# Kernel tuning notes

Hardware: AMD Instinct MI355X
Metric: run time of the kernel (lower is better)

Reference implementation:

```python
import jax, jax.numpy as jnp
import numpy as np

EPS = 1e-5

def layer_norm(x, gamma, beta):
    mu = jnp.mean(x, axis=-1, keepdims=True)
    var = jnp.var(x, axis=-1, keepdims=True)
    return (x - mu) * jax.lax.rsqrt(var + EPS) * gamma + beta

def setup_inputs() -> dict:
    key = jax.random.key(0)
    ks = jax.random.split(key, 8)
    T, B, E, H, K = 2048, 2, 1024, 16, 64
    x = jax.random.normal(ks[0], (T, B, E), dtype=jnp.float32)
    # causal mask: 0 where allowed (s<=t), -1e9 where masked
    attn_mask = jnp.where(jnp.tril(jnp.ones((T, T), dtype=bool)), 0.0, -1e9).astype(jnp.float32)
    def xavier(k, shape, gain):
        fan_out, fan_in = shape
        std = gain * np.sqrt(2.0 / (fan_in + fan_out))
        return (jax.random.normal(k, shape, dtype=jnp.float32) * std)
    Wq = xavier(ks[1], (H * K, E), 1.0)
    Wk = xavier(ks[2], (K, E), 1.0)
    Wv = xavier(ks[3], (E, E), 1.0)
    return {
        'x': x, 'attn_mask': attn_mask,
        'Wq': Wq, 'bq': jnp.zeros((H * K,), jnp.float32),
        'Wk': Wk, 'bk': jnp.zeros((K,), jnp.float32),
        'Wv': Wv, 'bv': jnp.zeros((E,), jnp.float32),
        'k_gamma': jnp.ones((K,), jnp.float32), 'k_beta': jnp.zeros((K,), jnp.float32),
        'v_gamma': jnp.ones((E,), jnp.float32), 'v_beta': jnp.zeros((E,), jnp.float32),
    }

def reference(x, attn_mask, Wq, bq, Wk, bk, Wv, bv, k_gamma, k_beta, v_gamma, v_beta):
    T, B, E = x.shape
    K = Wk.shape[0]
    H = Wq.shape[0] // K
    q = (x @ Wq.T + bq).reshape(T, B, H, K)          # [T,B,H,K]
    k = layer_norm(x @ Wk.T + bk, k_gamma, k_beta)   # [T,B,K]
    v = layer_norm(x @ Wv.T + bv, v_gamma, v_beta)   # [T,B,E]
    # outer-product state per step, then causal cumulative sum.
    # einsum('ts,sbkd->tbkd', scaling*causal_mask, s) == cumsum over s<=t,
    # scaled per query position t by (t+1)^-0.5 (mask is causal lower-tri).
    outer = jnp.einsum('tbk,tbd->tbkd', k, v)        # [T,B,K,E]
    s = jnp.cumsum(outer, axis=0)
    scaling = jax.lax.rsqrt(jnp.arange(1, T + 1, dtype=x.dtype))
    s = s * scaling[:, None, None, None]
    qn = jnp.mean(jax.nn.softmax(q, axis=-1), axis=2)  # [T,B,K] (dropout_p=0, eval)
    attn = jnp.einsum('tbk,tbkd->tbd', qn, s)          # [T,B,E]
    return attn
```

## Files before the change

### kernel.cpp

```cpp
#include <hip/hip_runtime.h>
#include <math.h>

#define T_DIM 2048
#define B_DIM 2
#define E_DIM 1024
#define K_DIM 64
#define H_DIM 16
#define R_DIM (T_DIM * B_DIM)
#define WROWS 2176
#define NCH 16

typedef __bf16 bf16x8 __attribute__((ext_vector_type(8)));
typedef __bf16 bf16x4 __attribute__((ext_vector_type(4)));
typedef float f32x4 __attribute__((ext_vector_type(4)));

#define GLD16(gptr, lptr)                                                      \
    __builtin_amdgcn_global_load_lds(                                          \
        (const __attribute__((address_space(1))) void*)(gptr),                 \
        (__attribute__((address_space(3))) void*)(lptr), 16, 0, 0)

__global__ __launch_bounds__(256) void cvt_all(const float* __restrict__ X,
                                               const float* __restrict__ Wq,
                                               const float* __restrict__ Wv,
                                               const float* __restrict__ Wk,
                                               __bf16* __restrict__ XB,
                                               __bf16* __restrict__ WB) {
    const size_t nq = (size_t)1024 * 1024;
    const size_t nk = (size_t)64 * 1024;
    bf16x8 o;
    if (blockIdx.x < 2048) {
        size_t g = ((size_t)blockIdx.x * 256 + threadIdx.x) * 8;
        float4 a = *(const float4*)&X[g];
        float4 b = *(const float4*)&X[g + 4];
        o[0] = (__bf16)a.x; o[1] = (__bf16)a.y; o[2] = (__bf16)a.z; o[3] = (__bf16)a.w;
        o[4] = (__bf16)b.x; o[5] = (__bf16)b.y; o[6] = (__bf16)b.z; o[7] = (__bf16)b.w;
        *(bf16x8*)&XB[g] = o;
    } else {
        size_t g = ((size_t)(blockIdx.x - 2048) * 256 + threadIdx.x) * 8;
        if (g < 2 * nq + nk) {
            const float* src;
            size_t off;
            if (g < nq)          { src = Wq; off = g; }
            else if (g < 2 * nq) { src = Wv; off = g - nq; }
            else                 { src = Wk; off = g - 2 * nq; }
            float4 a = *(const float4*)&src[off];
            float4 b = *(const float4*)&src[off + 4];
            o[0] = (__bf16)a.x; o[1] = (__bf16)a.y; o[2] = (__bf16)a.z; o[3] = (__bf16)a.w;
            o[4] = (__bf16)b.x; o[5] = (__bf16)b.y; o[6] = (__bf16)b.z; o[7] = (__bf16)b.w;
        } else {
#pragma unroll
            for (int i = 0; i < 8; ++i) o[i] = (__bf16)0.f;
        }
        *(bf16x8*)&WB[g] = o;
    }
}

__global__ __launch_bounds__(256) void gemm_mfma(const __bf16* __restrict__ XB,
                                                 const __bf16* __restrict__ WB,
                                                 const float* __restrict__ bq,
                                                 const float* __restrict__ bv,
                                                 const float* __restrict__ bk,
                                                 __bf16* __restrict__ Qb,
                                                 __bf16* __restrict__ Vb,
                                                 float* __restrict__ Kr) {
    __shared__ __bf16 Als[128 * 32];
    __shared__ __bf16 Bls[128 * 32];
    const int bid = blockIdx.x;
    const int v = (bid & 7) * 68 + (bid >> 3);
    const int bx = v / 17;
    const int by = v % 17;
    const int tid = threadIdx.x;
    const int lane = tid & 63;
    const int w = tid >> 6;
    const int wm = (w & 1) * 64;
    const int wn = (w >> 1) * 64;
    const int rBase = bx * 128;
    const int cBase = by * 128;

    const int c0 = tid, c1 = tid + 256;
    const __bf16* gA0 = XB + (size_t)(rBase + (c0 >> 2)) * E_DIM + (c0 & 3) * 8;
    const __bf16* gA1 = XB + (size_t)(rBase + (c1 >> 2)) * E_DIM + (c1 & 3) * 8;
    const __bf16* gB0 = WB + (size_t)(cBase + (c0 >> 2)) * E_DIM + (c0 & 3) * 8;
    const __bf16* gB1 = WB + (size_t)(cBase + (c1 >> 2)) * E_DIM + (c1 & 3) * 8;
    __bf16* lA0 = Als + c0 * 8;
    __bf16* lA1 = Als + c1 * 8;
    __bf16* lB0 = Bls + c0 * 8;
    __bf16* lB1 = Bls + c1 * 8;

    const int fr = lane & 15;
    const int fk = (lane >> 4) * 8;
    const __bf16* aF = Als + (wm + fr) * 32 + fk;
    const __bf16* bF = Bls + (wn + fr) * 32 + fk;

    f32x4 acc[4][4] = {};

    for (int kk = 0; kk < E_DIM; kk += 32) {
        __syncthreads();
        GLD16(gA0 + kk, lA0);
        GLD16(gA1 + kk, lA1);
        GLD16(gB0 + kk, lB0);
        GLD16(gB1 + kk, lB1);
        __syncthreads();

        bf16x8 af[4], bfr[4];
#pragma unroll
        for (int mt = 0; mt < 4; ++mt) af[mt] = *(const bf16x8*)(aF + mt * 16 * 32);
#pragma unroll
        for (int nt = 0; nt < 4; ++nt) bfr[nt] = *(const bf16x8*)(bF + nt * 16 * 32);
#pragma unroll
        for (int mt = 0; mt < 4; ++mt)
#pragma unroll
            for (int nt = 0; nt < 4; ++nt)
                acc[mt][nt] = __builtin_amdgcn_mfma_f32_16x16x32_bf16(
                    af[mt], bfr[nt], acc[mt][nt], 0, 0, 0);
    }

    const int row0 = rBase + wm + (lane >> 4) * 4;
    if (cBase < 2048) {
        const float* bias;
        __bf16* Cout;
        int colBase;
        if (cBase < 1024) { bias = bq; Cout = Qb; colBase = cBase; }
        else              { bias = bv; Cout = Vb; colBase = cBase - 1024; }
        const int col0 = colBase + wn + (lane & 15);
#pragma unroll
        for (int mt = 0; mt < 4; ++mt)
#pragma unroll
            for (int nt = 0; nt < 4; ++nt) {
                int cc = col0 + nt * 16;
                float bb = bias[cc];
#pragma unroll
                for (int r = 0; r < 4; ++r)
                    Cout[(size_t)(row0 + mt * 16 + r) * E_DIM + cc] =
                        (__bf16)(acc[mt][nt][r] + bb);
            }
    } else {
        const int col0 = wn + (lane & 15);
#pragma unroll
        for (int mt = 0; mt < 4; ++mt)
#pragma unroll
            for (int nt = 0; nt < 4; ++nt) {
                int cc = col0 + nt * 16;
                if (cc < 64) {
                    float bb = bk[cc];
#pragma unroll
                    for (int r = 0; r < 4; ++r)
                        Kr[(size_t)(row0 + mt * 16 + r) * K_DIM + cc] =
                            acc[mt][nt][r] + bb;
                }
            }
    }
}

__global__ __launch_bounds__(256) void rowops(const __bf16* __restrict__ Qb,
                                              const float* __restrict__ Kraw,
                                              const __bf16* __restrict__ Vb,
                                              const float* __restrict__ kg,
                                              const float* __restrict__ kb,
                                              __bf16* __restrict__ QNB,
                                              __bf16* __restrict__ KNB,
                                              float2* __restrict__ ST) {
    const int r = blockIdx.x;
    const int tid = threadIdx.x;
    const int lane = tid & 63, wv = tid >> 6;
    const int t = r >> 1, b = r & 1;
    __shared__ float redq[4][64];
    __shared__ float redv[2][4];

    float acc = 0.f;
#pragma unroll
    for (int h4 = 0; h4 < 4; ++h4) {
        int h = wv * 4 + h4;
        float v = (float)Qb[(size_t)r * 1024 + h * 64 + lane];
        float m = v;
#pragma unroll
        for (int off = 32; off; off >>= 1) m = fmaxf(m, __shfl_xor(m, off));
        float e = expf(v - m);
        float ssum = e;
#pragma unroll
        for (int off = 32; off; off >>= 1) ssum += __shfl_xor(ssum, off);
        acc += e / ssum;
    }
    redq[wv][lane] = acc;

    {
        bf16x4 v4 = *(const bf16x4*)&Vb[(size_t)r * 1024 + tid * 4];
        float a = (float)v4[0], c = (float)v4[1], d = (float)v4[2], e = (float)v4[3];
        float s = a + c + d + e;
        float s2 = a * a + c * c + d * d + e * e;
#pragma unroll
        for (int off = 32; off; off >>= 1) {
            s += __shfl_xor(s, off);
            s2 += __shfl_xor(s2, off);
        }
        if (lane == 0) { redv[0][wv] = s; redv[1][wv] = s2; }
    }
    __syncthreads();

    if (tid < 64) {
        float s = redq[0][tid] + redq[1][tid] + redq[2][tid] + redq[3][tid];
        QNB[((size_t)b * T_DIM + t) * K_DIM + tid] = (__bf16)(s * (1.f / 16.f));
    } else if (tid < 128) {
        float v = Kraw[(size_t)r * K_DIM + lane];
        float s = v, s2 = v * v;
#pragma unroll
        for (int off = 32; off; off >>= 1) {
            s += __shfl_xor(s, off);
            s2 += __shfl_xor(s2, off);
        }
        float mean = s * (1.f / 64.f);
        float var = s2 * (1.f / 64.f) - mean * mean;
        float inv = rsqrtf(var + 1e-5f);
        KNB[((size_t)b * T_DIM + t) * K_DIM + lane] =
            (__bf16)((v - mean) * inv * kg[lane] + kb[lane]);
    } else if (tid == 128) {
        float s = redv[0][0] + redv[0][1] + redv[0][2] + redv[0][3];
        float s2 = redv[1][0] + redv[1][1] + redv[1][2] + redv[1][3];
        float mean = s * (1.f / 1024.f);
        float var = s2 * (1.f / 1024.f) - mean * mean;
        ST[r] = make_float2(mean, rsqrtf(var + 1e-5f));
    }
}

__global__ __launch_bounds__(256) void lnT_stateU(const __bf16* __restrict__ VB,
                                                  const float2* __restrict__ ST,
                                                  const float* __restrict__ gamma,
                                                  const float* __restrict__ beta,
                                                  const __bf16* __restrict__ KNB,
                                                  __bf16* __restrict__ VT,
                                                  float* __restrict__ U) {
    __shared__ float tile[64][65];
    __shared__ __bf16 knT[64 * 136];
    __shared__ __bf16 VTl[64 * 136];
    const int c = blockIdx.x, b = blockIdx.y, eq = blockIdx.z;
    const int tid = threadIdx.x;
    const int lane = tid & 63;
    const int w = tid >> 6;
    const int fr = lane & 15;
    const int quad = lane >> 4;
    const int e0 = eq * 64;

    {
        int s = tid >> 1, kh = (tid & 1) * 32;
        const __bf16* src = KNB + ((size_t)b * T_DIM + c * 128 + s) * K_DIM + kh;
#pragma unroll
        for (int i8 = 0; i8 < 4; ++i8) {
            bf16x8 vv = *(const bf16x8*)&src[i8 * 8];
#pragma unroll
            for (int i = 0; i < 8; ++i) knT[(kh + i8 * 8 + i) * 136 + s] = vv[i];
        }
    }

#pragma unroll
    for (int th = 0; th < 2; ++th) {
#pragma unroll
        for (int j = 0; j < 2; ++j) {
            int idx = tid + j * 256;
            int tl = idx >> 3, e8 = idx & 7;
            int r = (c * 128 + th * 64 + tl) * B_DIM + b;
            float2 st = ST[r];
            bf16x8 vv = *(const bf16x8*)&VB[(size_t)r * E_DIM + e0 + e8 * 8];
#pragma unroll
            for (int i = 0; i < 8; ++i)
                tile[tl][e8 * 8 + i] = ((float)vv[i] - st.x) * st.y;
        }
        __syncthreads();
#pragma unroll
        for (int j = 0; j < 4; ++j) {
            int idx = tid + j * 256;
            int e = idx >> 4, t4 = idx & 15;
            float g = gamma[e0 + e], bb = beta[e0 + e];
            bf16x4 o;
#pragma unroll
            for (int i = 0; i < 4; ++i) o[i] = (__bf16)(tile[t4 * 4 + i][e] * g + bb);
            *(bf16x4*)&VT[((size_t)b * E_DIM + e0 + e) * T_DIM + c * 128 + th * 64 + t4 * 4] = o;
            *(bf16x4*)&VTl[e * 136 + th * 64 + t4 * 4] = o;
        }
        __syncthreads();
    }

    f32x4 acc[4] = {};
#pragma unroll
    for (int kit = 0; kit < 4; ++kit) {
        bf16x8 af = *(const bf16x8*)&VTl[(w * 16 + fr) * 136 + kit * 32 + quad * 8];
        bf16x8 bfr[4];
#pragma unroll
        for (int nt = 0; nt < 4; ++nt)
            bfr[nt] = *(const bf16x8*)&knT[(nt * 16 + fr) * 136 + kit * 32 + quad * 8];
#pragma unroll
        for (int nt = 0; nt < 4; ++nt)
            acc[nt] = __builtin_amdgcn_mfma_f32_16x16x32_bf16(
                af, bfr[nt], acc[nt], 0, 0, 0);
    }

    float* ub = U + ((size_t)(c * 2 + b) * 1024 + e0) * K_DIM;
#pragma unroll
    for (int nt = 0; nt < 4; ++nt) {
        int k = nt * 16 + fr;
#pragma unroll
        for (int r = 0; r < 4; ++r)
            ub[(size_t)(w * 16 + quad * 4 + r) * K_DIM + k] = acc[nt][r];
    }
}

__global__ __launch_bounds__(256) void scanS(const float* __restrict__ U,
                                             __bf16* __restrict__ Shi,
                                             __bf16* __restrict__ Slo) {
    const size_t idx = (size_t)blockIdx.x * 256 + threadIdx.x;
    float run = 0.f;
#pragma unroll
    for (int c = 0; c < NCH; ++c) {
        __bf16 h = (__bf16)run;
        Shi[(size_t)c * 131072 + idx] = h;
        Slo[(size_t)c * 131072 + idx] = (__bf16)(run - (float)h);
        run += U[(size_t)c * 131072 + idx];
    }
}

__global__ __launch_bounds__(256) void outPV(const __bf16* __restrict__ QNB,
                                             const __bf16* __restrict__ KNB,
                                             const __bf16* __restrict__ VT,
                                             const __bf16* __restrict__ Shi,
                                             const __bf16* __restrict__ Slo,
                                             float* __restrict__ OUT) {
    __shared__ __align__(16) __bf16 qns[128 * 72];
    __shared__ __align__(16) __bf16 Pl[128 * 136];
    __shared__ __align__(16) __bf16 Vls[128 * 32];
    const int c = blockIdx.x, b = blockIdx.y, eo = blockIdx.z;
    const int tid = threadIdx.x;
    const int lane = tid & 63;
    const int w = tid >> 6;
    const int fr = lane & 15;
    const int quad = lane >> 4;

#pragma unroll
    for (int j = 0; j < 4; ++j) {
        int idx = tid + j * 256;
        int row = idx >> 3, k8 = idx & 7;
        *(bf16x8*)&qns[row * 72 + k8 * 8] =
            *(const bf16x8*)&QNB[((size_t)b * T_DIM + c * 128 + row) * K_DIM + k8 * 8];
    }
    __syncthreads();

    const __bf16* knc = KNB + ((size_t)b * T_DIM + c * 128) * K_DIM;
    {
        f32x4 pacc[8][2] = {};
#pragma unroll
        for (int kit = 0; kit < 2; ++kit) {
            bf16x8 bq[2];
#pragma unroll
            for (int nt = 0; nt < 2; ++nt) {
                int q = w * 32 + nt * 16 + fr;
                bq[nt] = *(const bf16x8*)&qns[q * 72 + kit * 32 + quad * 8];
            }
#pragma unroll
            for (int mt = 0; mt < 8; ++mt) {
                bf16x8 af = *(const bf16x8*)&knc[(size_t)(mt * 16 + fr) * K_DIM +
                                                 kit * 32 + quad * 8];
#pragma unroll
                for (int nt = 0; nt < 2; ++nt)
                    pacc[mt][nt] = __builtin_amdgcn_mfma_f32_16x16x32_bf16(
                        af, bq[nt], pacc[mt][nt], 0, 0, 0);
            }
        }
#pragma unroll
        for (int mt = 0; mt < 8; ++mt)
#pragma unroll
            for (int nt = 0; nt < 2; ++nt) {
                int q = w * 32 + nt * 16 + fr;
                int s0 = mt * 16 + quad * 4;
                bf16x4 o;
#pragma unroll
                for (int r = 0; r < 4; ++r) {
                    float val = pacc[mt][nt][r];
                    if (s0 + r > q) val = 0.f;
                    o[r] = (__bf16)val;
                }
                *(bf16x4*)&Pl[q * 136 + s0] = o;
            }
    }
    __syncthreads();

    const int we = (w & 1) * 64, wt = (w >> 1) * 64;
    const int e0 = eo * 128;
    f32x4 acc[4][4] = {};

    if (c > 0) {
        const __bf16* sh = Shi + (size_t)c * 131072 + ((size_t)b * 1024 + e0 + we) * K_DIM;
        const __bf16* sl = Slo + (size_t)c * 131072 + ((size_t)b * 1024 + e0 + we) * K_DIM;
#pragma unroll
        for (int kit = 0; kit < 2; ++kit) {
            bf16x8 bq[4];
#pragma unroll
            for (int nt = 0; nt < 4; ++nt) {
                int t = wt + nt * 16 + fr;
                bq[nt] = *(const bf16x8*)&qns[t * 72 + kit * 32 + quad * 8];
            }
#pragma unroll
            for (int mt = 0; mt < 4; ++mt) {
                size_t ro = (size_t)(mt * 16 + fr) * K_DIM + kit * 32 + quad * 8;
                bf16x8 ah = *(const bf16x8*)&sh[ro];
                bf16x8 al = *(const bf16x8*)&sl[ro];
#pragma unroll
                for (int nt = 0; nt < 4; ++nt) {
                    acc[mt][nt] = __builtin_amdgcn_mfma_f32_16x16x32_bf16(
                        ah, bq[nt], acc[mt][nt], 0, 0, 0);
                    acc[mt][nt] = __builtin_amdgcn_mfma_f32_16x16x32_bf16(
                        al, bq[nt], acc[mt][nt], 0, 0, 0);
                }
            }
        }
    }

    const __bf16* vtb = VT + ((size_t)b * E_DIM + e0) * T_DIM + c * 128;
    for (int kit = 0; kit < 4; ++kit) {
        __syncthreads();
#pragma unroll
        for (int j = 0; j < 2; ++j) {
            int g = tid + j * 256;
            int row = g >> 2, part = g & 3;
            GLD16(vtb + (size_t)row * T_DIM + kit * 32 + part * 8, &Vls[g * 8]);
        }
        __syncthreads();
        bf16x8 av[4], bp[4];
#pragma unroll
        for (int mt = 0; mt < 4; ++mt)
            av[mt] = *(const bf16x8*)&Vls[(we + mt * 16 + fr) * 32 + quad * 8];
#pragma unroll
        for (int nt = 0; nt < 4; ++nt)
            bp[nt] = *(const bf16x8*)&Pl[(wt + nt * 16 + fr) * 136 + kit * 32 + quad * 8];
#pragma unroll
        for (int mt = 0; mt < 4; ++mt)
#pragma unroll
            for (int nt = 0; nt < 4; ++nt)
                acc[mt][nt] = __builtin_amdgcn_mfma_f32_16x16x32_bf16(
                    av[mt], bp[nt], acc[mt][nt], 0, 0, 0);
    }
    __syncthreads();

    float* tb = (float*)qns + w * 1280;
#pragma unroll
    for (int mt = 0; mt < 4; ++mt) {
#pragma unroll
        for (int nt = 0; nt < 4; ++nt)
            *(f32x4*)&tb[(nt * 16 + fr) * 20 + quad * 4] = acc[mt][nt];
#pragma unroll
        for (int j = 0; j < 4; ++j) {
            int fid = lane + j * 64;
            int trow = fid >> 2, e4 = fid & 3;
            float4 val = *(const float4*)&tb[trow * 20 + e4 * 4];
            int t = c * 128 + wt + trow;
            float sca = rsqrtf((float)(t + 1));
            float4 r = {val.x * sca, val.y * sca, val.z * sca, val.w * sca};
            *(float4*)&OUT[((size_t)t * B_DIM + b) * E_DIM + e0 + we + mt * 16 + e4 * 4] = r;
        }
    }
}

extern "C" void kernel_launch(void* const* d_in, const int* in_sizes, int n_in,
                              void* d_out, int out_size, void* d_ws,
                              size_t ws_size, hipStream_t stream) {
    const float* x = (const float*)d_in[0];
    const float* Wq = (const float*)d_in[2];
    const float* bq = (const float*)d_in[3];
    const float* Wk = (const float*)d_in[4];
    const float* bk = (const float*)d_in[5];
    const float* Wv = (const float*)d_in[6];
    const float* bv = (const float*)d_in[7];
    const float* kg = (const float*)d_in[8];
    const float* kb = (const float*)d_in[9];
    const float* vg = (const float*)d_in[10];
    const float* vb = (const float*)d_in[11];
    float* out = (float*)d_out;

    char* base = (char*)d_ws;
    const size_t MB = 1024 * 1024;
    __bf16* qb    = (__bf16*)(base + 0);
    __bf16* vbuf  = (__bf16*)(base + 8 * MB);
    float*  kraw  = (float*)(base + 16 * MB);
    __bf16* xb    = (__bf16*)(base + 17 * MB);
    __bf16* wb    = (__bf16*)(base + 25 * MB);
    __bf16* qnb   = (__bf16*)(base + 30 * MB);
    __bf16* knb   = (__bf16*)(base + 31 * MB);
    float2* stats = (float2*)(base + 32 * MB);
    float*  Ubuf = (float*)(base + 0);
    __bf16* Shi  = (__bf16*)(base + 8 * MB);
    __bf16* Slo  = (__bf16*)(base + 12 * MB);
    __bf16* vbT  = xb;

    cvt_all<<<dim3(2048 + WROWS * 1024 / 2048), 256, 0, stream>>>(x, Wq, Wv, Wk, xb, wb);
    gemm_mfma<<<dim3(544), 256, 0, stream>>>(xb, wb, bq, bv, bk, qb, vbuf, kraw);
    rowops<<<dim3(R_DIM), 256, 0, stream>>>(qb, kraw, vbuf, kg, kb, qnb, knb, stats);
    lnT_stateU<<<dim3(NCH, 2, 16), 256, 0, stream>>>(vbuf, stats, vg, vb, knb, vbT, Ubuf);
    scanS<<<dim3(512), 256, 0, stream>>>(Ubuf, Shi, Slo);
    outPV<<<dim3(NCH, 2, 8), 256, 0, stream>>>(qnb, knb, vbT, Shi, Slo, out);
}
```

Before: 172.7 us.

## Double-buffer LDS tiles in projection GEMM to overlap global loads with MFMA

The projection GEMM now keeps two LDS buffers for the A and B tiles. It issues the async global-to-LDS loads for the next K-slice before computing on the current one, using a manual vmcnt wait and raw barriers in place of the two syncthreads. The goal is to hide global memory latency behind the MFMA work. It doubles LDS use, which can lower occupancy, and correctness now depends on the hand-written vmcnt count matching the number of outstanding loads.

```diff
diff --git a/kernel.cpp b/kernel.cpp
--- a/kernel.cpp
+++ b/kernel.cpp
@@ -63,8 +63,8 @@
                                                  __bf16* __restrict__ Qb,
                                                  __bf16* __restrict__ Vb,
                                                  float* __restrict__ Kr) {
-    __shared__ __bf16 Als[128 * 32];
-    __shared__ __bf16 Bls[128 * 32];
+    __shared__ __bf16 Als[2][128 * 32];
+    __shared__ __bf16 Bls[2][128 * 32];
     const int bid = blockIdx.x;
     const int v = (bid & 7) * 68 + (bid >> 3);
     const int bx = v / 17;
@@ -82,38 +82,50 @@
     const __bf16* gA1 = XB + (size_t)(rBase + (c1 >> 2)) * E_DIM + (c1 & 3) * 8;
     const __bf16* gB0 = WB + (size_t)(cBase + (c0 >> 2)) * E_DIM + (c0 & 3) * 8;
     const __bf16* gB1 = WB + (size_t)(cBase + (c1 >> 2)) * E_DIM + (c1 & 3) * 8;
-    __bf16* lA0 = Als + c0 * 8;
-    __bf16* lA1 = Als + c1 * 8;
-    __bf16* lB0 = Bls + c0 * 8;
-    __bf16* lB1 = Bls + c1 * 8;
 
     const int fr = lane & 15;
     const int fk = (lane >> 4) * 8;
-    const __bf16* aF = Als + (wm + fr) * 32 + fk;
-    const __bf16* bF = Bls + (wn + fr) * 32 + fk;
 
     f32x4 acc[4][4] = {};
 
+#define STAGE(B, KK)                                                           \
+    {                                                                          \
+        GLD16(gA0 + (KK), &Als[B][c0 * 8]);                                    \
+        GLD16(gA1 + (KK), &Als[B][c1 * 8]);                                    \
+        GLD16(gB0 + (KK), &Bls[B][c0 * 8]);                                    \
+        GLD16(gB1 + (KK), &Bls[B][c1 * 8]);                                    \
+    }
+#define COMPUTE(B)                                                             \
+    {                                                                          \
+        const __bf16* aF = &Als[B][(wm + fr) * 32 + fk];                       \
+        const __bf16* bF = &Bls[B][(wn + fr) * 32 + fk];                       \
+        bf16x8 af[4], bfr[4];                                                  \
+        _Pragma("unroll") for (int mt = 0; mt < 4; ++mt)                       \
+            af[mt] = *(const bf16x8*)(aF + mt * 16 * 32);                      \
+        _Pragma("unroll") for (int nt = 0; nt < 4; ++nt)                       \
+            bfr[nt] = *(const bf16x8*)(bF + nt * 16 * 32);                     \
+        _Pragma("unroll") for (int mt = 0; mt < 4; ++mt)                       \
+            _Pragma("unroll") for (int nt = 0; nt < 4; ++nt)                   \
+                acc[mt][nt] = __builtin_amdgcn_mfma_f32_16x16x32_bf16(         \
+                    af[mt], bfr[nt], acc[mt][nt], 0, 0, 0);                    \
+    }
+
+    STAGE(0, 0);
+    int cur = 0;
     for (int kk = 0; kk < E_DIM; kk += 32) {
-        __syncthreads();
-        GLD16(gA0 + kk, lA0);
-        GLD16(gA1 + kk, lA1);
-        GLD16(gB0 + kk, lB0);
-        GLD16(gB1 + kk, lB1);
-        __syncthreads();
-
-        bf16x8 af[4], bfr[4];
-#pragma unroll
-        for (int mt = 0; mt < 4; ++mt) af[mt] = *(const bf16x8*)(aF + mt * 16 * 32);
-#pragma unroll
-        for (int nt = 0; nt < 4; ++nt) bfr[nt] = *(const bf16x8*)(bF + nt * 16 * 32);
-#pragma unroll
-        for (int mt = 0; mt < 4; ++mt)
-#pragma unroll
-            for (int nt = 0; nt < 4; ++nt)
-                acc[mt][nt] = __builtin_amdgcn_mfma_f32_16x16x32_bf16(
-                    af[mt], bfr[nt], acc[mt][nt], 0, 0, 0);
-    }
+        if (kk + 32 < E_DIM) {
+            STAGE(cur ^ 1, kk + 32);
+            asm volatile("s_waitcnt vmcnt(4)" ::: "memory");
+        } else {
+            asm volatile("s_waitcnt vmcnt(0)" ::: "memory");
+        }
+        __builtin_amdgcn_s_barrier();
+        COMPUTE(cur);
+        __builtin_amdgcn_s_barrier();
+        cur ^= 1;
+    }
+#undef STAGE
+#undef COMPUTE
 
     const int row0 = rBase + wm + (lane >> 4) * 4;
     if (cBase < 2048) {
```

Measured after the change: 176.0 us. Within noise of the previous version (+1.9%).
